# Kernel optimization log

Hardware: AMD Instinct MI355X
Metric: run time of the kernel (lower is better)

The kernel has to match this reference:

```python
import jax, jax.numpy as jnp
import numpy as np

POS_W = 1.0
ANG_W = 1.0
WID_W = 1.0
N = 1048560  # predictions (divisible by 17)
M = 8388480  # total GT grasps = sum(arange(N) % 17)


def setup_inputs() -> dict:
    key = jax.random.key(0)
    k1, k2 = jax.random.split(key)
    pred = jax.random.normal(k1, (N, 6), dtype=jnp.float32)
    all_targets = jax.random.normal(k2, (M, 6), dtype=jnp.float32)
    # ragged counts in [0, 16]; sum == M exactly
    target_counts = (jnp.arange(N, dtype=jnp.int64) % 17)
    return {"pred": pred, "all_targets": all_targets, "target_counts": target_counts}


def _smooth_l1(x):
    a = jnp.abs(x)
    return jnp.where(a < 1.0, 0.5 * x * x, a - 0.5)


def reference(pred, all_targets, target_counts):
    n = pred.shape[0]
    m = all_targets.shape[0]
    # segment id for each GT row (contiguous slices, order of target_counts)
    seg = jnp.repeat(jnp.arange(n), target_counts, total_repeat_length=m)  # (M,)
    p = pred[seg]  # (M,6) gathered predictions
    dp = p[:, :2] - all_targets[:, :2]
    da = p[:, 2:4] - all_targets[:, 2:4]
    dw = p[:, 4] - all_targets[:, 4]
    dist = (POS_W * jnp.sum(dp * dp, axis=-1)
            + ANG_W * jnp.sum(da * da, axis=-1)
            + WID_W * dw * dw)  # (M,)
    # ragged argmin per segment (first occurrence, like torch.argmin)
    min_d = jax.ops.segment_min(dist, seg, num_segments=n)  # (N,)
    row = jnp.arange(m)
    cand = jnp.where(dist == min_d[seg], row, m)
    arg = jax.ops.segment_min(cand, seg, num_segments=n)  # (N,) global row idx or m
    has = target_counts > 0
    gt = all_targets[jnp.where(has, jnp.clip(arg, 0, m - 1), 0)]  # (N,6)
    # fused per-prediction loss against the closest GT
    loss_pos = jnp.sum(_smooth_l1(pred[:, :2] - gt[:, :2]), axis=-1)
    loss_ang = jnp.sum(jnp.abs(pred[:, 2:4] - gt[:, 2:4]), axis=-1)
    loss_wid = _smooth_l1(pred[:, 4] - gt[:, 4])
    losses = jnp.where(has, POS_W * loss_pos + ANG_W * loss_ang + WID_W * loss_wid, 0.0)
    return jnp.mean(losses)  # reduction='mean'
```

## Files before the change

### kernel.cpp

```cpp
#include <hip/hip_runtime.h>
#include <math.h>

#define POS_W 1.0f
#define ANG_W 1.0f
#define WID_W 1.0f

__device__ __forceinline__ float smooth_l1(float x) {
    float a = fabsf(x);
    return a < 1.0f ? 0.5f * x * x : a - 0.5f;
}

__global__ void k_block_sums(const int* __restrict__ counts, int stride, int n,
                             int* __restrict__ blockSums) {
    int i = blockIdx.x * 256 + threadIdx.x;
    int c = (i < n) ? counts[(long long)i * stride] : 0;
    for (int off = 32; off > 0; off >>= 1) c += __shfl_down(c, off, 64);
    __shared__ int sdata[4];
    int lane = threadIdx.x & 63, wave = threadIdx.x >> 6;
    if (lane == 0) sdata[wave] = c;
    __syncthreads();
    if (threadIdx.x == 0)
        blockSums[blockIdx.x] = sdata[0] + sdata[1] + sdata[2] + sdata[3];
}

__global__ void k_scan_blocks(const int* __restrict__ blockSums, int nb,
                              int* __restrict__ blockOffs) {
    int t = threadIdx.x;
    int per = (nb + 255) / 256;
    int start = t * per;
    int end = min(start + per, nb);
    int sum = 0;
    for (int j = start; j < end; ++j) sum += blockSums[j];
    __shared__ int s[256];
    s[t] = sum;
    __syncthreads();
    for (int d = 1; d < 256; d <<= 1) {
        int v = (t >= d) ? s[t - d] : 0;
        __syncthreads();
        s[t] += v;
        __syncthreads();
    }
    int run = s[t] - sum;
    for (int j = start; j < end; ++j) {
        blockOffs[j] = run;
        run += blockSums[j];
    }
}

__global__ void k_loss(const float* __restrict__ pred,
                       const float* __restrict__ tgt,
                       const int* __restrict__ counts, int stride, int n,
                       const int* __restrict__ blockOffs, float invN,
                       float* __restrict__ out) {
    int t = threadIdx.x;
    int i = blockIdx.x * 256 + t;
    int c = (i < n) ? counts[(long long)i * stride] : 0;

    __shared__ int s[256];
    s[t] = c;
    __syncthreads();
    for (int d = 1; d < 256; d <<= 1) {
        int v = (t >= d) ? s[t - d] : 0;
        __syncthreads();
        s[t] += v;
        __syncthreads();
    }
    int off = blockOffs[blockIdx.x] + s[t] - c;

    float loss = 0.0f;
    if (i < n && c > 0) {
        const float* p = pred + (long long)i * 6;
        float p0 = p[0], p1 = p[1], p2 = p[2], p3 = p[3], p4 = p[4];
        float best = INFINITY;
        float b0 = 0, b1 = 0, b2 = 0, b3 = 0, b4 = 0;
        const float* g = tgt + (long long)off * 6;
        for (int k = 0; k < c; ++k) {
            float g0 = g[0], g1 = g[1], g2 = g[2], g3 = g[3], g4 = g[4];
            float d0 = p0 - g0, d1 = p1 - g1, d2 = p2 - g2, d3 = p3 - g3,
                  d4 = p4 - g4;
            float dist = POS_W * (d0 * d0 + d1 * d1) +
                         ANG_W * (d2 * d2 + d3 * d3) + WID_W * d4 * d4;
            if (dist < best) {
                best = dist;
                b0 = g0; b1 = g1; b2 = g2; b3 = g3; b4 = g4;
            }
            g += 6;
        }
        loss = POS_W * (smooth_l1(p0 - b0) + smooth_l1(p1 - b1)) +
               ANG_W * (fabsf(p2 - b2) + fabsf(p3 - b3)) +
               WID_W * smooth_l1(p4 - b4);
    }

    for (int o = 32; o > 0; o >>= 1) loss += __shfl_down(loss, o, 64);
    __shared__ float fs[4];
    int lane = t & 63, wave = t >> 6;
    if (lane == 0) fs[wave] = loss;
    __syncthreads();
    if (t == 0) {
        float tot = (fs[0] + fs[1] + fs[2] + fs[3]) * invN;
        atomicAdd(out, tot);
    }
}

extern "C" void kernel_launch(void* const* d_in, const int* in_sizes, int n_in,
                              void* d_out, int out_size, void* d_ws,
                              size_t ws_size, hipStream_t stream) {
    const float* pred = (const float*)d_in[0];
    const float* tgt = (const float*)d_in[1];
    const int* counts = (const int*)d_in[2];
    int n = in_sizes[0] / 6;
    int stride = (in_sizes[2] == n) ? 1 : 2;
    int nb = (n + 255) / 256;

    int* blockSums = (int*)d_ws;
    int* blockOffs = blockSums + nb;
    float* out = (float*)d_out;

    hipMemsetAsync(d_out, 0, sizeof(float), stream);
    k_block_sums<<<nb, 256, 0, stream>>>(counts, stride, n, blockSums);
    k_scan_blocks<<<1, 256, 0, stream>>>(blockSums, nb, blockOffs);
    k_loss<<<nb, 256, 0, stream>>>(pred, tgt, counts, stride, n, blockOffs,
                                   1.0f / n, out);
}
```

Baseline: 356.4 us.

## Stage block's target window through shared memory with coalesced float2 loads

Each block now copies its contiguous window of target rows into LDS in chunks of 1024 rows, using coalesced float2 loads across all threads. Each thread then scans its own segment from shared memory instead of walking strided global rows one at a time. Prediction rows are also read as float2. The intent is to replace uncoalesced per-thread global reads with cooperative coalesced ones. The cost is about 24KB of LDS per block, which may limit occupancy, plus extra barriers per chunk.

```diff
diff --git a/kernel.cpp b/kernel.cpp
--- a/kernel.cpp
+++ b/kernel.cpp
@@ -4,6 +4,7 @@
 #define POS_W 1.0f
 #define ANG_W 1.0f
 #define WID_W 1.0f
+#define CHUNK 1024
 
 __device__ __forceinline__ float smooth_l1(float x) {
     float a = fabsf(x);
@@ -47,16 +48,17 @@
     }
 }
 
-__global__ void k_loss(const float* __restrict__ pred,
-                       const float* __restrict__ tgt,
-                       const int* __restrict__ counts, int stride, int n,
-                       const int* __restrict__ blockOffs, float invN,
-                       float* __restrict__ out) {
+__global__ __launch_bounds__(256) void k_loss(
+    const float* __restrict__ pred, const float* __restrict__ tgt,
+    const int* __restrict__ counts, int stride, int n,
+    const int* __restrict__ blockOffs, float invN, float* __restrict__ out) {
+    __shared__ int s[256];
+    __shared__ float2 ch[CHUNK * 3];
+
     int t = threadIdx.x;
     int i = blockIdx.x * 256 + t;
     int c = (i < n) ? counts[(long long)i * stride] : 0;
 
-    __shared__ int s[256];
     s[t] = c;
     __syncthreads();
     for (int d = 1; d < 256; d <<= 1) {
@@ -65,27 +67,48 @@
         s[t] += v;
         __syncthreads();
     }
-    int off = blockOffs[blockIdx.x] + s[t] - c;
+    int off = s[t] - c;
+    int total = s[255];
+    int winStart = blockOffs[blockIdx.x];
+
+    bool active = (i < n) && (c > 0);
+    float p0 = 0, p1 = 0, p2 = 0, p3 = 0, p4 = 0;
+    if (active) {
+        const float2* p2p = (const float2*)(pred + (long long)i * 6);
+        float2 a = p2p[0], b = p2p[1], w = p2p[2];
+        p0 = a.x; p1 = a.y; p2 = b.x; p3 = b.y; p4 = w.x;
+    }
+
+    float best = INFINITY;
+    float b0 = 0, b1 = 0, b2 = 0, b3 = 0, b4 = 0;
+
+    const float2* tgt2 = (const float2*)tgt;
+    for (int base = 0; base < total; base += CHUNK) {
+        int rows = min(CHUNK, total - base);
+        const float2* src = tgt2 + (long long)(winStart + base) * 3;
+        for (int k = t; k < rows * 3; k += 256) ch[k] = src[k];
+        __syncthreads();
+        if (active) {
+            int lo = max(off, base), hi = min(off + c, base + rows);
+            for (int r = lo; r < hi; ++r) {
+                int l3 = (r - base) * 3;
+                float2 ga = ch[l3], gb = ch[l3 + 1], gw = ch[l3 + 2];
+                float d0 = p0 - ga.x, d1 = p1 - ga.y;
+                float d2 = p2 - gb.x, d3 = p3 - gb.y;
+                float d4 = p4 - gw.x;
+                float dist = POS_W * (d0 * d0 + d1 * d1) +
+                             ANG_W * (d2 * d2 + d3 * d3) + WID_W * d4 * d4;
+                if (dist < best) {
+                    best = dist;
+                    b0 = ga.x; b1 = ga.y; b2 = gb.x; b3 = gb.y; b4 = gw.x;
+                }
+            }
+        }
+        __syncthreads();
+    }
 
     float loss = 0.0f;
-    if (i < n && c > 0) {
-        const float* p = pred + (long long)i * 6;
-        float p0 = p[0], p1 = p[1], p2 = p[2], p3 = p[3], p4 = p[4];
-        float best = INFINITY;
-        float b0 = 0, b1 = 0, b2 = 0, b3 = 0, b4 = 0;
-        const float* g = tgt + (long long)off * 6;
-        for (int k = 0; k < c; ++k) {
-            float g0 = g[0], g1 = g[1], g2 = g[2], g3 = g[3], g4 = g[4];
-            float d0 = p0 - g0, d1 = p1 - g1, d2 = p2 - g2, d3 = p3 - g3,
-                  d4 = p4 - g4;
-            float dist = POS_W * (d0 * d0 + d1 * d1) +
-                         ANG_W * (d2 * d2 + d3 * d3) + WID_W * d4 * d4;
-            if (dist < best) {
-                best = dist;
-                b0 = g0; b1 = g1; b2 = g2; b3 = g3; b4 = g4;
-            }
-            g += 6;
-        }
+    if (active) {
         loss = POS_W * (smooth_l1(p0 - b0) + smooth_l1(p1 - b1)) +
                ANG_W * (fabsf(p2 - b2) + fabsf(p3 - b3)) +
                WID_W * smooth_l1(p4 - b4);
```

Result: faster. 339.2 us (-4.8%).
